# Kernel tuning notes

Measured on AMD Instinct MI355X. Metric: run time of the kernel, lower is better.

The kernel has to match this reference:

```python
import jax, jax.numpy as jnp
import numpy as np

N, E, D_IN, D_H = 50000, 800000, 128, 128


def setup_inputs() -> dict:
    key = jax.random.key(0)
    ks = jax.random.split(key, 8)
    x = jax.random.normal(ks[0], (N, D_IN), dtype=jnp.float32)
    edge_index = jax.random.randint(ks[1], (2, E), 0, N, dtype=jnp.int64)
    edge_attr = jax.random.normal(ks[2], (E, D_H), dtype=jnp.float32)
    s_in = 1.0 / np.sqrt(D_IN)
    W_mean = jax.random.uniform(ks[3], (D_H, D_IN), jnp.float32, -s_in, s_in)
    b_mean = jax.random.uniform(ks[4], (D_H,), jnp.float32, -s_in, s_in)
    W_std = jax.random.uniform(ks[5], (D_H, D_IN), jnp.float32, -s_in, s_in)
    b_std = jax.random.uniform(ks[6], (D_H,), jnp.float32, -s_in, s_in)
    return {"x": x, "edge_index": edge_index, "edge_attr": edge_attr,
            "W_mean": W_mean, "b_mean": b_mean, "W_std": W_std, "b_std": b_std}


def _gcn(x, edge_index, edge_attr, W, b):
    # linear projection: [N, D_H]
    h = x @ W.T + b
    row, col = edge_index[0], edge_index[1]
    n = x.shape[0]
    # degree of target nodes (col), symmetric-ish normalization
    deg = jax.ops.segment_sum(jnp.ones(row.shape[0], dtype=h.dtype), col, num_segments=n)
    deg_inv_sqrt = jnp.where(deg > 0, jax.lax.rsqrt(jnp.maximum(deg, 1.0)) * jnp.where(deg > 0, 1.0, 0.0), 0.0)
    norm = deg_inv_sqrt[row] * deg_inv_sqrt[col]  # [E]
    msg = norm[:, None] * (h[row] + edge_attr)     # [E, D_H]
    out = jax.ops.segment_sum(msg, col, num_segments=n) + h  # aggregate at target + residual
    return out


def reference(x, edge_index, edge_attr, W_mean, b_mean, W_std, b_std):
    mean = _gcn(x, edge_index, edge_attr, W_mean, b_mean)
    std = _gcn(x, edge_index, edge_attr, W_std, b_std)
    return (mean, std)
```

## Files before the change

### kernel.cpp

```cpp
#include <hip/hip_runtime.h>
#include <math.h>

#define N_NODES 50000
#define N_EDGES 800000
#define D 128

typedef float        vf2 __attribute__((ext_vector_type(2)));
typedef unsigned int vu2 __attribute__((ext_vector_type(2)));
typedef int          vi4 __attribute__((ext_vector_type(4)));

static __device__ __forceinline__ unsigned short f2bf(float f) {
    unsigned u = __float_as_uint(f);
    u += 0x7FFFu + ((u >> 16) & 1u);
    return (unsigned short)(u >> 16);
}

__global__ __launch_bounds__(256) void hist_kernel(const int* __restrict__ ei,
                                                   int* __restrict__ count) {
    int e = blockIdx.x * blockDim.x + threadIdx.x;
    if (e < N_EDGES) {
        atomicAdd(&count[ei[N_EDGES + e]], 1);
    }
}

__global__ __launch_bounds__(1024) void scan1_kernel(const int* __restrict__ count,
                                                     int* __restrict__ offset,
                                                     float* __restrict__ dis,
                                                     int* __restrict__ bsum) {
    __shared__ int wsum[16];
    const int tid = threadIdx.x;
    const int lane = tid & 63;
    const int wid = tid >> 6;
    const int i = blockIdx.x * 1024 + tid;

    int c = (i < N_NODES) ? count[i] : 0;
    int inc = c;
#pragma unroll
    for (int d = 1; d < 64; d <<= 1) {
        int v = __shfl_up(inc, d, 64);
        if (lane >= d) inc += v;
    }
    if (lane == 63) wsum[wid] = inc;
    __syncthreads();
    if (wid == 0) {
        int s = (lane < 16) ? wsum[lane] : 0;
#pragma unroll
        for (int d = 1; d < 16; d <<= 1) {
            int v = __shfl_up(s, d, 64);
            if (lane >= d) s += v;
        }
        if (lane < 16) wsum[lane] = s;
    }
    __syncthreads();
    int wpre = (wid > 0) ? wsum[wid - 1] : 0;
    if (i < N_NODES) {
        offset[i] = wpre + inc - c;
        dis[i] = (c > 0) ? rsqrtf((float)c) : 0.0f;
    }
    if (tid == 0) bsum[blockIdx.x] = wsum[15];
}

__global__ __launch_bounds__(1024) void fixup_kernel(const int* __restrict__ bsum,
                                                     int* __restrict__ offset,
                                                     int* __restrict__ cur) {
    __shared__ int pre_s;
    const int tid = threadIdx.x;
    const int blk = blockIdx.x;
    if ((tid >> 6) == 0) {
        int lane = tid & 63;
        int s = 0;
        for (int j = lane; j < blk; j += 64) s += bsum[j];
#pragma unroll
        for (int d = 32; d > 0; d >>= 1) s += __shfl_xor(s, d, 64);
        if (lane == 0) pre_s = s;
    }
    __syncthreads();
    int i = blk * 1024 + tid;
    if (i < N_NODES) {
        int o = offset[i] + pre_s;
        offset[i] = o;
        cur[i] = o;
    }
}

#define TILE_R 32
#define GEMM_BLKS ((N_NODES + TILE_R - 1) / TILE_R)
#define SCAT_BLKS ((N_EDGES + 255) / 256)
__global__ __launch_bounds__(256) void fused_kernel(
    const float* __restrict__ x,
    const float* __restrict__ Wm, const float* __restrict__ bm,
    const float* __restrict__ Ws, const float* __restrict__ bs,
    float* __restrict__ h, ushort2* __restrict__ hpk,
    const int* __restrict__ ei, const float* __restrict__ dis,
    int* __restrict__ cur, int4* __restrict__ meta)
{
    __shared__ float xs[TILE_R][D];
    const int tid = threadIdx.x;

    if (blockIdx.x >= GEMM_BLKS) {
        int e = (blockIdx.x - GEMM_BLKS) * 256 + tid;
        if (e < N_EDGES) {
            int row = ei[e];
            int col = ei[N_EDGES + e];
            int p = atomicAdd(&cur[col], 1);
            meta[p] = make_int4(e, row, __float_as_int(dis[row]), 0);
        }
        return;
    }

    const int r0 = blockIdx.x * TILE_R;

    for (int i = tid; i < TILE_R * D / 4; i += 256) {
        int rr = i / (D / 4);
        int cc = (i % (D / 4)) * 4;
        int r = r0 + rr;
        float4 v = make_float4(0.f, 0.f, 0.f, 0.f);
        if (r < N_NODES) v = *(const float4*)(x + (size_t)r * D + cc);
        *(float4*)(&xs[rr][cc]) = v;
    }
    __syncthreads();

    const int m = tid >> 7;
    const int p = (tid >> 1) & 63;
    const int rh = tid & 1;
    const int c0 = p * 2;
    const float* __restrict__ W = m ? Ws : Wm;
    const float* __restrict__ b = m ? bs : bm;
    const float b0 = b[c0], b1 = b[c0 + 1];

    float acc0[16], acc1[16];
#pragma unroll
    for (int rr = 0; rr < 16; ++rr) { acc0[rr] = b0; acc1[rr] = b1; }

    const float* __restrict__ Wr0 = W + (size_t)c0 * D;
    const float* __restrict__ Wr1 = W + (size_t)(c0 + 1) * D;

    for (int kc = 0; kc < D; kc += 32) {
        float w0[32], w1[32];
#pragma unroll
        for (int j = 0; j < 32; j += 4) {
            float4 a = *(const float4*)(Wr0 + kc + j);
            float4 bb = *(const float4*)(Wr1 + kc + j);
            w0[j] = a.x; w0[j+1] = a.y; w0[j+2] = a.z; w0[j+3] = a.w;
            w1[j] = bb.x; w1[j+1] = bb.y; w1[j+2] = bb.z; w1[j+3] = bb.w;
        }
#pragma unroll
        for (int rr = 0; rr < 16; ++rr) {
            const float* xr = &xs[rh * 16 + rr][kc];
#pragma unroll
            for (int j = 0; j < 32; j += 4) {
                float4 xv = *(const float4*)(xr + j);
                acc0[rr] = fmaf(xv.x, w0[j],     acc0[rr]);
                acc0[rr] = fmaf(xv.y, w0[j + 1], acc0[rr]);
                acc0[rr] = fmaf(xv.z, w0[j + 2], acc0[rr]);
                acc0[rr] = fmaf(xv.w, w0[j + 3], acc0[rr]);
                acc1[rr] = fmaf(xv.x, w1[j],     acc1[rr]);
                acc1[rr] = fmaf(xv.y, w1[j + 1], acc1[rr]);
                acc1[rr] = fmaf(xv.z, w1[j + 2], acc1[rr]);
                acc1[rr] = fmaf(xv.w, w1[j + 3], acc1[rr]);
            }
        }
    }

    const size_t hb = (size_t)m * N_NODES * D;
#pragma unroll
    for (int rr = 0; rr < 16; ++rr) {
        int r = r0 + rh * 16 + rr;
        if (r < N_NODES) {
            float2 v; v.x = acc0[rr]; v.y = acc1[rr];
            *(float2*)(h + hb + (size_t)r * D + c0) = v;
            ushort2 u; u.x = f2bf(acc0[rr]); u.y = f2bf(acc1[rr]);
            hpk[(size_t)r * 128 + p * 2 + m] = u;
        }
    }
}

__global__ __launch_bounds__(256) void agg_kernel(
    const float* __restrict__ ea, const vu2* __restrict__ hpk,
    const int4* __restrict__ meta,
    const int* __restrict__ offset, const int* __restrict__ cur,
    const float* __restrict__ dis,
    const float* __restrict__ hm, const float* __restrict__ hs,
    float* __restrict__ om, float* __restrict__ os)
{
    const int tid = threadIdx.x;
    const int lane = tid & 63;
    const int wid = tid >> 6;
    const int n = blockIdx.x * 4 + wid;

    const int start = offset[n];
    const int end = cur[n];
    const float dc = dis[n];
    const int k = lane * 2;

    const size_t ob = (size_t)n * D + k;
    vf2 hmn = __builtin_nontemporal_load((const vf2*)(hm + ob));
    vf2 hsn = __builtin_nontemporal_load((const vf2*)(hs + ob));

    float amx = 0.f, amy = 0.f, asx = 0.f, asy = 0.f;

    for (int jb = start; jb < end; jb += 64) {
        vi4 mt = (vi4)(0);
        if (jb + lane < end)
            mt = __builtin_nontemporal_load((const vi4*)(meta + jb + lane));
        const int mm = min(64, end - jb);

        int   eA = __builtin_amdgcn_readlane(mt[0], 0);
        int   rA = __builtin_amdgcn_readlane(mt[1], 0);
        float dA = __int_as_float(__builtin_amdgcn_readlane(mt[2], 0));
        vf2 eaA = __builtin_nontemporal_load((const vf2*)(ea + (size_t)eA * D + k));
        vu2 hpA = hpk[(size_t)rA * 64 + lane];

        const int j1 = (mm > 1) ? 1 : 0;
        int   eB = __builtin_amdgcn_readlane(mt[0], j1);
        int   rB = __builtin_amdgcn_readlane(mt[1], j1);
        float dB = __int_as_float(__builtin_amdgcn_readlane(mt[2], j1));
        vf2 eaB = __builtin_nontemporal_load((const vf2*)(ea + (size_t)eB * D + k));
        vu2 hpB = hpk[(size_t)rB * 64 + lane];

        for (int j = 0; j < mm; ++j) {
            const int jn = (j + 2 < mm) ? (j + 2) : (mm - 1);
            int   eN = __builtin_amdgcn_readlane(mt[0], jn);
            int   rN = __builtin_amdgcn_readlane(mt[1], jn);
            float dN = __int_as_float(__builtin_amdgcn_readlane(mt[2], jn));
            vf2 eaN = __builtin_nontemporal_load((const vf2*)(ea + (size_t)eN * D + k));
            vu2 hpN = hpk[(size_t)rN * 64 + lane];

            float h0 = __uint_as_float(hpA[0] << 16);
            float h1 = __uint_as_float(hpA[0] & 0xFFFF0000u);
            float g0 = __uint_as_float(hpA[1] << 16);
            float g1 = __uint_as_float(hpA[1] & 0xFFFF0000u);

            amx = fmaf(dA, h0 + eaA[0], amx);
            amy = fmaf(dA, h1 + eaA[1], amy);
            asx = fmaf(dA, g0 + eaA[0], asx);
            asy = fmaf(dA, g1 + eaA[1], asy);

            eaA = eaB; hpA = hpB; dA = dB;
            eaB = eaN; hpB = hpN; dB = dN;
        }
    }

    vf2 o0, o1;
    o0[0] = hmn[0] + dc * amx;  o0[1] = hmn[1] + dc * amy;
    o1[0] = hsn[0] + dc * asx;  o1[1] = hsn[1] + dc * asy;
    __builtin_nontemporal_store(o0, (vf2*)(om + ob));
    __builtin_nontemporal_store(o1, (vf2*)(os + ob));
}

extern "C" void kernel_launch(void* const* d_in, const int* in_sizes, int n_in,
                              void* d_out, int out_size, void* d_ws, size_t ws_size,
                              hipStream_t stream) {
    const float* x   = (const float*)d_in[0];
    const int*   ei  = (const int*)d_in[1];
    const float* ea  = (const float*)d_in[2];
    const float* Wm  = (const float*)d_in[3];
    const float* bm  = (const float*)d_in[4];
    const float* Ws  = (const float*)d_in[5];
    const float* bs  = (const float*)d_in[6];
    float* out = (float*)d_out;

    char* w = (char*)d_ws;
    int*   count  = (int*)w;     w += (size_t)N_NODES * 4;
    int*   offset = (int*)w;     w += (size_t)N_NODES * 4;
    int*   cur    = (int*)w;     w += (size_t)N_NODES * 4;
    float* dis    = (float*)w;   w += (size_t)N_NODES * 4;
    int*   bsum   = (int*)w;     w += 4096;
    int4*  meta   = (int4*)w;    w += (size_t)N_EDGES * 16;
    float* h      = (float*)w;   w += (size_t)2 * N_NODES * D * 4;
    ushort2* hpk  = (ushort2*)w;
    float* hm = h;
    float* hs = h + (size_t)N_NODES * D;

    float* om = out;
    float* os = out + (size_t)N_NODES * D;

    const int SCAN_BLKS = (N_NODES + 1023) / 1024;

    hipMemsetAsync(count, 0, N_NODES * sizeof(int), stream);

    hist_kernel<<<SCAT_BLKS, 256, 0, stream>>>(ei, count);

    scan1_kernel<<<SCAN_BLKS, 1024, 0, stream>>>(count, offset, dis, bsum);
    fixup_kernel<<<SCAN_BLKS, 1024, 0, stream>>>(bsum, offset, cur);

    fused_kernel<<<GEMM_BLKS + SCAT_BLKS, 256, 0, stream>>>(
        x, Wm, bm, Ws, bs, h, hpk, ei, dis, cur, meta);

    agg_kernel<<<N_NODES / 4, 256, 0, stream>>>(ea, (const vu2*)hpk, meta,
                                                offset, cur, dis, hm, hs, om, os);
}
```

Baseline: 267.8 us.

## Split GEMM across hist and scatter kernels, drop fp32 h, compact meta

Splits the projection GEMM tiles between the histogram kernel and the scatter kernel so each overlaps with atomic work. The fp32 h buffer is no longer written; the residual is read back from the packed bf16 copy. Edge metadata shrinks from 16 to 8 bytes by packing the row index with a bf16 norm factor. The aggregation loop is unrolled 4-way with deeper prefetch. This cuts memory traffic but makes the residual and norm bf16-precision, and packing row into 16 bits breaks for node indices at or above 65536 (N=50000 fits).

New measurement: 302.0 us. +12.8%, slower.

```diff
diff --git a/kernel.cpp b/kernel.cpp
--- a/kernel.cpp
+++ b/kernel.cpp
@@ -5,110 +5,30 @@
 #define N_EDGES 800000
 #define D 128
 
+#define TILE_R 32
+#define HIST_BLKS ((N_EDGES + 255) / 256)
+#define SCAT_BLKS HIST_BLKS
+#define GEMM_BLKS ((N_NODES + TILE_R - 1) / TILE_R)
+#define GEMM_A (GEMM_BLKS / 2)
+#define GEMM_B (GEMM_BLKS - GEMM_A)
+
 typedef float        vf2 __attribute__((ext_vector_type(2)));
 typedef unsigned int vu2 __attribute__((ext_vector_type(2)));
-typedef int          vi4 __attribute__((ext_vector_type(4)));
-
-static __device__ __forceinline__ unsigned short f2bf(float f) {
+
+static __device__ __forceinline__ unsigned f2bf(float f) {
     unsigned u = __float_as_uint(f);
     u += 0x7FFFu + ((u >> 16) & 1u);
-    return (unsigned short)(u >> 16);
-}
-
-__global__ __launch_bounds__(256) void hist_kernel(const int* __restrict__ ei,
-                                                   int* __restrict__ count) {
-    int e = blockIdx.x * blockDim.x + threadIdx.x;
-    if (e < N_EDGES) {
-        atomicAdd(&count[ei[N_EDGES + e]], 1);
-    }
-}
-
-__global__ __launch_bounds__(1024) void scan1_kernel(const int* __restrict__ count,
-                                                     int* __restrict__ offset,
-                                                     float* __restrict__ dis,
-                                                     int* __restrict__ bsum) {
-    __shared__ int wsum[16];
-    const int tid = threadIdx.x;
-    const int lane = tid & 63;
-    const int wid = tid >> 6;
-    const int i = blockIdx.x * 1024 + tid;
-
-    int c = (i < N_NODES) ? count[i] : 0;
-    int inc = c;
-#pragma unroll
-    for (int d = 1; d < 64; d <<= 1) {
-        int v = __shfl_up(inc, d, 64);
-        if (lane >= d) inc += v;
-    }
-    if (lane == 63) wsum[wid] = inc;
-    __syncthreads();
-    if (wid == 0) {
-        int s = (lane < 16) ? wsum[lane] : 0;
-#pragma unroll
-        for (int d = 1; d < 16; d <<= 1) {
-            int v = __shfl_up(s, d, 64);
-            if (lane >= d) s += v;
-        }
-        if (lane < 16) wsum[lane] = s;
-    }
-    __syncthreads();
-    int wpre = (wid > 0) ? wsum[wid - 1] : 0;
-    if (i < N_NODES) {
-        offset[i] = wpre + inc - c;
-        dis[i] = (c > 0) ? rsqrtf((float)c) : 0.0f;
-    }
-    if (tid == 0) bsum[blockIdx.x] = wsum[15];
-}
-
-__global__ __launch_bounds__(1024) void fixup_kernel(const int* __restrict__ bsum,
-                                                     int* __restrict__ offset,
-                                                     int* __restrict__ cur) {
-    __shared__ int pre_s;
-    const int tid = threadIdx.x;
-    const int blk = blockIdx.x;
-    if ((tid >> 6) == 0) {
-        int lane = tid & 63;
-        int s = 0;
-        for (int j = lane; j < blk; j += 64) s += bsum[j];
-#pragma unroll
-        for (int d = 32; d > 0; d >>= 1) s += __shfl_xor(s, d, 64);
-        if (lane == 0) pre_s = s;
-    }
-    __syncthreads();
-    int i = blk * 1024 + tid;
-    if (i < N_NODES) {
-        int o = offset[i] + pre_s;
-        offset[i] = o;
-        cur[i] = o;
-    }
-}
-
-#define TILE_R 32
-#define GEMM_BLKS ((N_NODES + TILE_R - 1) / TILE_R)
-#define SCAT_BLKS ((N_EDGES + 255) / 256)
-__global__ __launch_bounds__(256) void fused_kernel(
+    return u >> 16;
+}
+
+static __device__ __forceinline__ void gemm_tile(
+    int r0, int tid,
     const float* __restrict__ x,
     const float* __restrict__ Wm, const float* __restrict__ bm,
     const float* __restrict__ Ws, const float* __restrict__ bs,
-    float* __restrict__ h, ushort2* __restrict__ hpk,
-    const int* __restrict__ ei, const float* __restrict__ dis,
-    int* __restrict__ cur, int4* __restrict__ meta)
+    unsigned* __restrict__ hpk)
 {
     __shared__ float xs[TILE_R][D];
-    const int tid = threadIdx.x;
-
-    if (blockIdx.x >= GEMM_BLKS) {
-        int e = (blockIdx.x - GEMM_BLKS) * 256 + tid;
-        if (e < N_EDGES) {
-            int row = ei[e];
-            int col = ei[N_EDGES + e];
-            int p = atomicAdd(&cur[col], 1);
-            meta[p] = make_int4(e, row, __float_as_int(dis[row]), 0);
-        }
-        return;
-    }
-
-    const int r0 = blockIdx.x * TILE_R;
 
     for (int i = tid; i < TILE_R * D / 4; i += 256) {
         int rr = i / (D / 4);
@@ -162,25 +82,154 @@
         }
     }
 
-    const size_t hb = (size_t)m * N_NODES * D;
 #pragma unroll
     for (int rr = 0; rr < 16; ++rr) {
         int r = r0 + rh * 16 + rr;
         if (r < N_NODES) {
-            float2 v; v.x = acc0[rr]; v.y = acc1[rr];
-            *(float2*)(h + hb + (size_t)r * D + c0) = v;
-            ushort2 u; u.x = f2bf(acc0[rr]); u.y = f2bf(acc1[rr]);
-            hpk[(size_t)r * 128 + p * 2 + m] = u;
-        }
-    }
-}
-
-__global__ __launch_bounds__(256) void agg_kernel(
-    const float* __restrict__ ea, const vu2* __restrict__ hpk,
-    const int4* __restrict__ meta,
+            unsigned word = f2bf(acc0[rr]) | (f2bf(acc1[rr]) << 16);
+            hpk[(size_t)r * 128 + p * 2 + m] = word;
+        }
+    }
+}
+
+__global__ __launch_bounds__(256) void k1_hist_gemm(
+    const int* __restrict__ ei, int* __restrict__ count,
+    const float* __restrict__ x,
+    const float* __restrict__ Wm, const float* __restrict__ bm,
+    const float* __restrict__ Ws, const float* __restrict__ bs,
+    unsigned* __restrict__ hpk)
+{
+    if (blockIdx.x < HIST_BLKS) {
+        int e = blockIdx.x * 256 + threadIdx.x;
+        if (e < N_EDGES) atomicAdd(&count[ei[N_EDGES + e]], 1);
+        return;
+    }
+    gemm_tile((blockIdx.x - HIST_BLKS) * TILE_R, threadIdx.x,
+              x, Wm, bm, Ws, bs, hpk);
+}
+
+__global__ __launch_bounds__(1024) void scan1_kernel(const int* __restrict__ count,
+                                                     int* __restrict__ offset,
+                                                     float* __restrict__ dis,
+                                                     int* __restrict__ bsum) {
+    __shared__ int wsum[16];
+    const int tid = threadIdx.x;
+    const int lane = tid & 63;
+    const int wid = tid >> 6;
+    const int i = blockIdx.x * 1024 + tid;
+
+    int c = (i < N_NODES) ? count[i] : 0;
+    int inc = c;
+#pragma unroll
+    for (int d = 1; d < 64; d <<= 1) {
+        int v = __shfl_up(inc, d, 64);
+        if (lane >= d) inc += v;
+    }
+    if (lane == 63) wsum[wid] = inc;
+    __syncthreads();
+    if (wid == 0) {
+        int s = (lane < 16) ? wsum[lane] : 0;
+#pragma unroll
+        for (int d = 1; d < 16; d <<= 1) {
+            int v = __shfl_up(s, d, 64);
+            if (lane >= d) s += v;
+        }
+        if (lane < 16) wsum[lane] = s;
+    }
+    __syncthreads();
+    int wpre = (wid > 0) ? wsum[wid - 1] : 0;
+    if (i < N_NODES) {
+        offset[i] = wpre + inc - c;
+        dis[i] = (c > 0) ? rsqrtf((float)c) : 0.0f;
+    }
+    if (tid == 0) bsum[blockIdx.x] = wsum[15];
+}
+
+__global__ __launch_bounds__(1024) void fixup_kernel(const int* __restrict__ bsum,
+                                                     int* __restrict__ offset,
+                                                     int* __restrict__ cur) {
+    __shared__ int pre_s;
+    const int tid = threadIdx.x;
+    const int blk = blockIdx.x;
+    if ((tid >> 6) == 0) {
+        int lane = tid & 63;
+        int s = 0;
+        for (int j = lane; j < blk; j += 64) s += bsum[j];
+#pragma unroll
+        for (int d = 32; d > 0; d >>= 1) s += __shfl_xor(s, d, 64);
+        if (lane == 0) pre_s = s;
+    }
+    __syncthreads();
+    int i = blk * 1024 + tid;
+    if (i < N_NODES) {
+        int o = offset[i] + pre_s;
+        offset[i] = o;
+        cur[i] = o;
+    }
+}
+
+__global__ __launch_bounds__(256) void k4_scat_gemm(
+    const int* __restrict__ ei, const float* __restrict__ dis,
+    int* __restrict__ cur, vu2* __restrict__ meta,
+    const float* __restrict__ x,
+    const float* __restrict__ Wm, const float* __restrict__ bm,
+    const float* __restrict__ Ws, const float* __restrict__ bs,
+    unsigned* __restrict__ hpk)
+{
+    if (blockIdx.x < SCAT_BLKS) {
+        int e = blockIdx.x * 256 + threadIdx.x;
+        if (e < N_EDGES) {
+            int row = ei[e];
+            int col = ei[N_EDGES + e];
+            int p = atomicAdd(&cur[col], 1);
+            vu2 v;
+            v[0] = (unsigned)e;
+            v[1] = (unsigned)row | (f2bf(dis[row]) << 16);
+            meta[p] = v;
+        }
+        return;
+    }
+    gemm_tile((GEMM_A + (int)blockIdx.x - SCAT_BLKS) * TILE_R, threadIdx.x,
+              x, Wm, bm, Ws, bs, hpk);
+}
+
+#define STEP(u)                                                                 \
+    {                                                                           \
+        float h0 = __uint_as_float(hp##u[0] << 16);                             \
+        float h1 = __uint_as_float(hp##u[0] & 0xFFFF0000u);                     \
+        float g0 = __uint_as_float(hp##u[1] << 16);                             \
+        float g1 = __uint_as_float(hp##u[1] & 0xFFFF0000u);                     \
+        amx = fmaf(dr##u, h0 + ea##u[0], amx);                                  \
+        amy = fmaf(dr##u, h1 + ea##u[1], amy);                                  \
+        asx = fmaf(dr##u, g0 + ea##u[0], asx);                                  \
+        asy = fmaf(dr##u, g1 + ea##u[1], asy);                                  \
+        int jn = j + u + 4;                                                     \
+        int jj = (jn < mm) ? jn : mm - 1;                                       \
+        unsigned ev = (unsigned)__builtin_amdgcn_readlane((int)mt[0], jj);      \
+        unsigned pk = (unsigned)__builtin_amdgcn_readlane((int)mt[1], jj);      \
+        ea##u = __builtin_nontemporal_load(                                     \
+            (const vf2*)(eap + (size_t)ev * D + k));                            \
+        hp##u = hpk[(size_t)(pk & 0xFFFFu) * 64 + lane];                        \
+        dr##u = (jn < mm) ? __uint_as_float(pk & 0xFFFF0000u) : 0.0f;           \
+    }
+
+#define PRIME(u)                                                                \
+    float dr##u; vf2 ea##u; vu2 hp##u;                                          \
+    {                                                                           \
+        int jj = (u < mm) ? u : mm - 1;                                         \
+        unsigned ev = (unsigned)__builtin_amdgcn_readlane((int)mt[0], jj);      \
+        unsigned pk = (unsigned)__builtin_amdgcn_readlane((int)mt[1], jj);      \
+        ea##u = __builtin_nontemporal_load(                                     \
+            (const vf2*)(eap + (size_t)ev * D + k));                            \
+        hp##u = hpk[(size_t)(pk & 0xFFFFu) * 64 + lane];                        \
+        dr##u = (u < mm) ? __uint_as_float(pk & 0xFFFF0000u) : 0.0f;            \
+    }
+
+__global__ __launch_bounds__(256, 8) void agg_kernel(
+    const float* __restrict__ eap, const vu2* __restrict__ hpk,
+    const vu2* __restrict__ meta,
     const int* __restrict__ offset, const int* __restrict__ cur,
     const float* __restrict__ dis,
-    const float* __restrict__ hm, const float* __restrict__ hs,
     float* __restrict__ om, float* __restrict__ os)
 {
     const int tid = threadIdx.x;
@@ -193,57 +242,29 @@
     const float dc = dis[n];
     const int k = lane * 2;
 
+    vu2 hpn = hpk[(size_t)n * 64 + lane];
+
+    float amx = 0.f, amy = 0.f, asx = 0.f, asy = 0.f;
+
+    for (int jb = start; jb < end; jb += 64) {
+        vu2 mt = (vu2)(0);
+        if (jb + lane < end)
+            mt = __builtin_nontemporal_load(meta + jb + lane);
+        const int mm = min(64, end - jb);
+
+        PRIME(0) PRIME(1) PRIME(2) PRIME(3)
+
+        for (int j = 0; j < mm; j += 4) {
+            STEP(0) STEP(1) STEP(2) STEP(3)
+        }
+    }
+
     const size_t ob = (size_t)n * D + k;
-    vf2 hmn = __builtin_nontemporal_load((const vf2*)(hm + ob));
-    vf2 hsn = __builtin_nontemporal_load((const vf2*)(hs + ob));
-
-    float amx = 0.f, amy = 0.f, asx = 0.f, asy = 0.f;
-
-    for (int jb = start; jb < end; jb += 64) {
-        vi4 mt = (vi4)(0);
-        if (jb + lane < end)
-            mt = __builtin_nontemporal_load((const vi4*)(meta + jb + lane));
-        const int mm = min(64, end - jb);
-
-        int   eA = __builtin_amdgcn_readlane(mt[0], 0);
-        int   rA = __builtin_amdgcn_readlane(mt[1], 0);
-        float dA = __int_as_float(__builtin_amdgcn_readlane(mt[2], 0));
-        vf2 eaA = __builtin_nontemporal_load((const vf2*)(ea + (size_t)eA * D + k));
-        vu2 hpA = hpk[(size_t)rA * 64 + lane];
-
-        const int j1 = (mm > 1) ? 1 : 0;
-        int   eB = __builtin_amdgcn_readlane(mt[0], j1);
-        int   rB = __builtin_amdgcn_readlane(mt[1], j1);
-        float dB = __int_as_float(__builtin_amdgcn_readlane(mt[2], j1));
-        vf2 eaB = __builtin_nontemporal_load((const vf2*)(ea + (size_t)eB * D + k));
-        vu2 hpB = hpk[(size_t)rB * 64 + lane];
-
-        for (int j = 0; j < mm; ++j) {
-            const int jn = (j + 2 < mm) ? (j + 2) : (mm - 1);
-            int   eN = __builtin_amdgcn_readlane(mt[0], jn);
-            int   rN = __builtin_amdgcn_readlane(mt[1], jn);
-            float dN = __int_as_float(__builtin_amdgcn_readlane(mt[2], jn));
-            vf2 eaN = __builtin_nontemporal_load((const vf2*)(ea + (size_t)eN * D + k));
-            vu2 hpN = hpk[(size_t)rN * 64 + lane];
-
-            float h0 = __uint_as_float(hpA[0] << 16);
-            float h1 = __uint_as_float(hpA[0] & 0xFFFF0000u);
-            float g0 = __uint_as_float(hpA[1] << 16);
-            float g1 = __uint_as_float(hpA[1] & 0xFFFF0000u);
-
-            amx = fmaf(dA, h0 + eaA[0], amx);
-            amy = fmaf(dA, h1 + eaA[1], amy);
-            asx = fmaf(dA, g0 + eaA[0], asx);
-            asy = fmaf(dA, g1 + eaA[1], asy);
-
-            eaA = eaB; hpA = hpB; dA = dB;
-            eaB = eaN; hpB = hpN; dB = dN;
-        }
-    }
-
     vf2 o0, o1;
-    o0[0] = hmn[0] + dc * amx;  o0[1] = hmn[1] + dc * amy;
-    o1[0] = hsn[0] + dc * asx;  o1[1] = hsn[1] + dc * asy;
+    o0[0] = __uint_as_float(hpn[0] << 16)         + dc * amx;
+    o0[1] = __uint_as_float(hpn[0] & 0xFFFF0000u) + dc * amy;
+    o1[0] = __uint_as_float(hpn[1] << 16)         + dc * asx;
+    o1[1] = __uint_as_float(hpn[1] & 0xFFFF0000u) + dc * asy;
     __builtin_nontemporal_store(o0, (vf2*)(om + ob));
     __builtin_nontemporal_store(o1, (vf2*)(os + ob));
 }
@@ -266,12 +287,8 @@
     int*   cur    = (int*)w;     w += (size_t)N_NODES * 4;
     float* dis    = (float*)w;   w += (size_t)N_NODES * 4;
     int*   bsum   = (int*)w;     w += 4096;
-    int4*  meta   = (int4*)w;    w += (size_t)N_EDGES * 16;
-    float* h      = (float*)w;   w += (size_t)2 * N_NODES * D * 4;
-    ushort2* hpk  = (ushort2*)w;
-    float* hm = h;
-    float* hs = h + (size_t)N_NODES * D;
-
+    vu2*   meta   = (vu2*)w;     w += (size_t)N_EDGES * 8;
+    unsigned* hpk = (unsigned*)w;
     float* om = out;
     float* os = out + (size_t)N_NODES * D;
 
@@ -279,14 +296,15 @@
 
     hipMemsetAsync(count, 0, N_NODES * sizeof(int), stream);
 
-    hist_kernel<<<SCAT_BLKS, 256, 0, stream>>>(ei, count);
+    k1_hist_gemm<<<HIST_BLKS + GEMM_A, 256, 0, stream>>>(
+        ei, count, x, Wm, bm, Ws, bs, hpk);
 
     scan1_kernel<<<SCAN_BLKS, 1024, 0, stream>>>(count, offset, dis, bsum);
     fixup_kernel<<<SCAN_BLKS, 1024, 0, stream>>>(bsum, offset, cur);
 
-    fused_kernel<<<GEMM_BLKS + SCAT_BLKS, 256, 0, stream>>>(
-        x, Wm, bm, Ws, bs, h, hpk, ei, dis, cur, meta);
-
-    agg_kernel<<<N_NODES / 4, 256, 0, stream>>>(ea, (const vu2*)hpk, meta,
-                                                offset, cur, dis, hm, hs, om, os);
-}
+    k4_scat_gemm<<<SCAT_BLKS + GEMM_B, 256, 0, stream>>>(
+        ei, dis, cur, meta, x, Wm, bm, Ws, bs, hpk);
+
+    agg_kernel<<<N_NODES / 4, 256, 0, stream>>>(
+        ea, (const vu2*)hpk, meta, offset, cur, dis, om, os);
+}
```
